# Performance work log

Measured on AMD Instinct MI355X. Metric: run time of the kernel, lower is better.

Reference implementation:

```python
import jax, jax.numpy as jnp
import numpy as np
from jax.experimental.ode import odeint

DIM = 768
BATCH = 2048
T = 32
W_SCALE = 0.02  # small init so dynamics are smooth for the adaptive solver


def setup_inputs() -> dict:
    key = jax.random.key(0)
    k = jax.random.split(key, 8)
    f32 = jnp.float32
    return {
        "x": jax.random.normal(k[0], (BATCH, DIM), f32),
        "t_span": (jnp.arange(T, dtype=f32) * 0.1),  # monotone increasing time grid
        # dynamics_net: Linear(dim, 2*dim) -> tanh -> Linear(2*dim, dim)
        "W1": jax.random.normal(k[1], (DIM, 2 * DIM), f32) * W_SCALE,
        "b1": jnp.zeros((2 * DIM,), f32),
        "W2": jax.random.normal(k[2], (2 * DIM, DIM), f32) * W_SCALE,
        "b2": jnp.zeros((DIM,), f32),
        # memory_net: Linear(dim, dim) -> tanh
        "Wm": jax.random.normal(k[3], (DIM, DIM), f32) * W_SCALE,
        "bm": jnp.zeros((DIM,), f32),
    }


def reference(x, t_span, W1, b1, W2, b2, Wm, bm):
    """Adaptive dopri5 integration of dE/dt = dynamics_net(E) + memory_net(E).

    Returns the emotional trajectory with shape [time, batch, dim], matching
    torchdiffeq.odeint(..., method='dopri5').
    """

    def f(y, t, W1, b1, W2, b2, Wm, bm):
        # dynamics_net(y): tanh MLP 768 -> 1536 -> 768
        dyn = jnp.tanh(y @ W1 + b1) @ W2 + b2
        # memory_net(y): tanh(Linear(768 -> 768))
        mem = jnp.tanh(y @ Wm + bm)
        return dyn + mem

    # jax's odeint is an adaptive dopri5 solver (same scheme as torchdiffeq dopri5).
    traj = odeint(f, x, t_span, W1, b1, W2, b2, Wm, bm, rtol=1e-5, atol=1e-6)
    return traj  # [T, BATCH, DIM]
```

## Files before the change

### kernel.cpp

```cpp
#include <hip/hip_runtime.h>
#include <math.h>

#define DIM   768
#define HID   1536
#define NCAT  2304
#define BATCH 2048
#define NELEM (BATCH * DIM)

typedef _Float16 f16x8 __attribute__((ext_vector_type(8)));
typedef _Float16 f16x4 __attribute__((ext_vector_type(4)));
typedef float f32x4 __attribute__((ext_vector_type(4)));

__device__ __forceinline__ float fast_tanh(float x) {
  float e = __expf(2.0f * x);
  return 1.0f - 2.0f / (e + 1.0f);
}

#define AS1 __attribute__((address_space(1)))
#define AS3 __attribute__((address_space(3)))
__device__ __forceinline__ void gload_lds16(const void* g, void* l) {
  __builtin_amdgcn_global_load_lds((const AS1 unsigned int*)g,
                                   (AS3 unsigned int*)l, 16, 0, 0);
}

template <int ROWS>
__device__ __forceinline__ void stage_tile(const _Float16* __restrict__ g,
                                           int K, char* lds, int w, int l) {
  constexpr int NCH = ROWS / 8;
  const int sub  = l >> 3;
  const int slot = (l & 7) ^ sub;
#pragma unroll
  for (int i = 0; i < NCH / 4; ++i) {
    const int j = w + i * 4;
    const int row = j * 8 + sub;
    gload_lds16(g + (size_t)row * K + slot * 8, lds + j * 1024);
  }
}

__device__ __forceinline__ f16x8 ldfrag(const char* base, int row, int kk,
                                        int lq) {
  const int slot = (kk * 4 + lq) ^ (row & 7);
  return *reinterpret_cast<const f16x8*>(base + row * 128 + slot * 16);
}

template <int MODE, int BM, int BN, int KITERS>
__global__ __launch_bounds__(256, (MODE == 0) ? 3 : 2) void gemm_k(
    const _Float16* __restrict__ A, const _Float16* __restrict__ Bt,
    const float* __restrict__ bias, _Float16* __restrict__ Hout,
    float* __restrict__ kmem, const float* __restrict__ b2,
    float* __restrict__ y, float* __restrict__ accb,
    _Float16* __restrict__ ts, float* __restrict__ out_row,
    const float* __restrict__ tg, int step, float hmul, int initf) {
  constexpr int K = KITERS * 64;
  constexpr int WM = BM / 32;
  constexpr int WN = BN / 32;
  constexpr int BUF = (BM + BN) * 128;
  constexpr int NBUF = (MODE == 0) ? 2 : 3;
  constexpr int SISS = BM / 32 + BN / 32;
  __shared__ __align__(16) char smem[NBUF * BUF];

  const int tid = threadIdx.x;
  const int w = tid >> 6, l = tid & 63;
  const int lr = l & 15, lq = l >> 4;
  const int m0 = blockIdx.y * BM;
  const int n0 = blockIdx.x * BN;
  const int wr = (w >> 1) * (WM * 16);
  const int wc = (w & 1) * (WN * 16);

  const _Float16* Ag = A + (size_t)m0 * K;
  const _Float16* Bg = Bt + (size_t)n0 * K;

  f32x4 acc[WM][WN];
#pragma unroll
  for (int m = 0; m < WM; ++m)
#pragma unroll
    for (int n = 0; n < WN; ++n) acc[m][n] = f32x4{0.f, 0.f, 0.f, 0.f};

  auto STAGE = [&](int t) {
    char* base = smem + (t % NBUF) * BUF;
    stage_tile<BM>(Ag + t * 64, K, base, w, l);
    stage_tile<BN>(Bg + t * 64, K, base + BM * 128, w, l);
  };

  STAGE(0);
  if (NBUF == 3 && KITERS > 1) STAGE(1);

  for (int kt = 0; kt < KITERS; ++kt) {
    if (NBUF == 2 && kt + 1 < KITERS) STAGE(kt + 1);
    if (kt + 1 < KITERS)
      asm volatile("s_waitcnt vmcnt(%0)" ::"n"(SISS) : "memory");
    else
      asm volatile("s_waitcnt vmcnt(0)" ::: "memory");
    __builtin_amdgcn_s_barrier();
    __builtin_amdgcn_sched_barrier(0);
    if (NBUF == 3 && kt + 2 < KITERS) STAGE(kt + 2);

    const char* As = smem + (kt % NBUF) * BUF;
    const char* Bs = As + BM * 128;
#pragma unroll
    for (int kk = 0; kk < 2; ++kk) {
      f16x8 afr[WM], bfr[WN];
#pragma unroll
      for (int n = 0; n < WN; ++n) bfr[n] = ldfrag(Bs, wc + n * 16 + lr, kk, lq);
#pragma unroll
      for (int m = 0; m < WM; ++m) afr[m] = ldfrag(As, wr + m * 16 + lr, kk, lq);
      __builtin_amdgcn_s_setprio(1);
#pragma unroll
      for (int m = 0; m < WM; ++m)
#pragma unroll
        for (int n = 0; n < WN; ++n)
          acc[m][n] = __builtin_amdgcn_mfma_f32_16x16x32_f16(afr[m], bfr[n],
                                                             acc[m][n], 0, 0, 0);
      __builtin_amdgcn_s_setprio(0);
    }
    if (NBUF == 2) __builtin_amdgcn_s_barrier();
  }

  if (MODE == 0) {
#pragma unroll
    for (int m = 0; m < WM; ++m)
#pragma unroll
      for (int n = 0; n < WN; ++n) {
        const int gcol = n0 + wc + n * 16 + lr;
        const float bv = bias[gcol];
#pragma unroll
        for (int j = 0; j < 4; ++j) {
          const int grow = m0 + wr + m * 16 + lq * 4 + j;
          const float t = fast_tanh(acc[m][n][j] + bv);
          if (gcol < HID)
            Hout[(size_t)grow * HID + gcol] = (_Float16)t;
          else
            kmem[(size_t)grow * DIM + (gcol - HID)] = t;
        }
      }
  } else {
    const float h = tg[step + 1] - tg[step];
#pragma unroll
    for (int m = 0; m < WM; ++m)
#pragma unroll
      for (int n = 0; n < WN; ++n) {
        const int gcol = n0 + wc + n * 16 + lr;
        const float bv = b2[gcol];
#pragma unroll
        for (int j = 0; j < 4; ++j) {
          const int grow = m0 + wr + m * 16 + lq * 4 + j;
          const size_t idx = (size_t)grow * DIM + gcol;
          const float kv = acc[m][n][j] + kmem[idx] + bv;
          if (MODE == 1) {
            const float av = initf ? kv : (accb[idx] + 2.0f * kv);
            accb[idx] = av;
            const float tv = y[idx] + (hmul * h) * kv;
            ts[idx] = (_Float16)tv;
          } else {
            const float v = y[idx] + (h * (1.0f / 6.0f)) * (accb[idx] + kv);
            y[idx] = v;
            out_row[idx] = v;
            ts[idx] = (_Float16)v;
          }
        }
      }
  }
}

__global__ __launch_bounds__(256) void init_k(
    const float* __restrict__ x, float* __restrict__ y,
    float* __restrict__ out0, _Float16* __restrict__ ys) {
  const int i4 = blockIdx.x * 256 + threadIdx.x;
  const int base = i4 * 4;
  f32x4 v = *(const f32x4*)(x + base);
  *(f32x4*)(y + base) = v;
  *(f32x4*)(out0 + base) = v;
  f16x4 hv;
#pragma unroll
  for (int j = 0; j < 4; ++j) hv[j] = (_Float16)v[j];
  *(f16x4*)(ys + base) = hv;
}

__global__ __launch_bounds__(256) void prep_wcat_k(
    const float* __restrict__ W1, const float* __restrict__ Wm,
    _Float16* __restrict__ out) {
  const int idx = blockIdx.x * 256 + threadIdx.x;
  const int nrow = idx / DIM, k = idx % DIM;
  const float v = (nrow < HID) ? W1[(size_t)k * HID + nrow]
                               : Wm[(size_t)k * DIM + (nrow - HID)];
  out[idx] = (_Float16)v;
}
__global__ __launch_bounds__(256) void prep_w2t_k(
    const float* __restrict__ W2, _Float16* __restrict__ out) {
  const int idx = blockIdx.x * 256 + threadIdx.x;
  const int nrow = idx / HID, k = idx % HID;
  out[idx] = (_Float16)W2[(size_t)k * DIM + nrow];
}
__global__ __launch_bounds__(256) void prep_bias_k(
    const float* __restrict__ b1, const float* __restrict__ bmv,
    float* __restrict__ out) {
  const int i = blockIdx.x * 256 + threadIdx.x;
  if (i < NCAT) out[i] = (i < HID) ? b1[i] : bmv[i - HID];
}

extern "C" void kernel_launch(void* const* d_in, const int* in_sizes, int n_in,
                              void* d_out, int out_size, void* d_ws,
                              size_t ws_size, hipStream_t stream) {
  const float* x  = (const float*)d_in[0];
  const float* tg = (const float*)d_in[1];
  const float* W1 = (const float*)d_in[2];
  const float* b1 = (const float*)d_in[3];
  const float* W2 = (const float*)d_in[4];
  const float* b2 = (const float*)d_in[5];
  const float* Wm = (const float*)d_in[6];
  const float* bm = (const float*)d_in[7];
  float* out = (float*)d_out;
  const int T = in_sizes[1];

  float* y        = (float*)d_ws;
  float* accb     = y + NELEM;
  float* kmem     = accb + NELEM;
  float* bias_cat = kmem + NELEM;
  _Float16* ys    = (_Float16*)(bias_cat + NCAT);
  _Float16* ts    = ys + NELEM;
  _Float16* Hh    = ts + NELEM;
  _Float16* WcatT = Hh + (size_t)BATCH * HID;
  _Float16* W2T   = WcatT + (size_t)NCAT * DIM;

  prep_wcat_k<<<(NCAT * DIM) / 256, 256, 0, stream>>>(W1, Wm, WcatT);
  prep_w2t_k<<<(DIM * HID) / 256, 256, 0, stream>>>(W2, W2T);
  prep_bias_k<<<(NCAT + 255) / 256, 256, 0, stream>>>(b1, bm, bias_cat);
  init_k<<<NELEM / 1024, 256, 0, stream>>>(x, y, out, ys);

  const dim3 g0(NCAT / 96, BATCH / 64);
  const dim3 g1(DIM / 96, BATCH / 32);

  auto gemm0 = [&](const _Float16* a) {
    gemm_k<0, 64, 96, 12><<<g0, 256, 0, stream>>>(
        a, WcatT, bias_cat, Hh, kmem, nullptr, nullptr, nullptr, nullptr,
        nullptr, nullptr, 0, 0.f, 0);
  };
  auto gemm1_stage = [&](int step, float hmul, int initf) {
    gemm_k<1, 32, 96, 24><<<g1, 256, 0, stream>>>(
        Hh, W2T, nullptr, nullptr, kmem, b2, y, accb, ts, nullptr, tg, step,
        hmul, initf);
  };
  auto gemm1_final = [&](int step, float* orow) {
    gemm_k<2, 32, 96, 24><<<g1, 256, 0, stream>>>(
        Hh, W2T, nullptr, nullptr, kmem, b2, y, accb, ys, orow, tg, step, 0.f,
        0);
  };

  for (int i = 0; i < T - 1; ++i) {
    gemm0(ys);  gemm1_stage(i, 0.5f, 1);
    gemm0(ts);  gemm1_stage(i, 0.5f, 0);
    gemm0(ts);  gemm1_stage(i, 1.0f, 0);
    gemm0(ts);  gemm1_final(i, out + (size_t)(i + 1) * NELEM);
  }
}
```

Before: 4.178 ms.

## Store kmem/accb in fp16, remap blocks per XCD, enlarge second GEMM tile

```diff
diff --git a/kernel.cpp b/kernel.cpp
--- a/kernel.cpp
+++ b/kernel.cpp
@@ -44,11 +44,11 @@
 }
 
 template <int MODE, int BM, int BN, int KITERS>
-__global__ __launch_bounds__(256, (MODE == 0) ? 3 : 2) void gemm_k(
+__global__ __launch_bounds__(256, (MODE == 0) ? 3 : 1) void gemm_k(
     const _Float16* __restrict__ A, const _Float16* __restrict__ Bt,
     const float* __restrict__ bias, _Float16* __restrict__ Hout,
-    float* __restrict__ kmem, const float* __restrict__ b2,
-    float* __restrict__ y, float* __restrict__ accb,
+    _Float16* __restrict__ kmem, const float* __restrict__ b2,
+    float* __restrict__ y, _Float16* __restrict__ accb,
     _Float16* __restrict__ ts, float* __restrict__ out_row,
     const float* __restrict__ tg, int step, float hmul, int initf) {
   constexpr int K = KITERS * 64;
@@ -62,8 +62,19 @@
   const int tid = threadIdx.x;
   const int w = tid >> 6, l = tid & 63;
   const int lr = l & 15, lq = l >> 4;
-  const int m0 = blockIdx.y * BM;
-  const int n0 = blockIdx.x * BN;
+
+  const int flat = blockIdx.x;
+  const int xcd = flat & 7, slot = flat >> 3;
+  int mt, nt;
+  if (MODE == 0) {
+    mt = (xcd & 1) * 16 + (slot & 15);
+    nt = (xcd >> 1) * 6 + (slot >> 4);
+  } else {
+    mt = (xcd & 3) * 8 + (slot & 7);
+    nt = (xcd >> 2) * 4 + (slot >> 3);
+  }
+  const int m0 = mt * BM;
+  const int n0 = nt * BN;
   const int wr = (w >> 1) * (WM * 16);
   const int wc = (w & 1) * (WN * 16);
 
@@ -130,7 +141,7 @@
           if (gcol < HID)
             Hout[(size_t)grow * HID + gcol] = (_Float16)t;
           else
-            kmem[(size_t)grow * DIM + (gcol - HID)] = t;
+            kmem[(size_t)grow * DIM + (gcol - HID)] = (_Float16)t;
         }
       }
   } else {
@@ -145,14 +156,15 @@
         for (int j = 0; j < 4; ++j) {
           const int grow = m0 + wr + m * 16 + lq * 4 + j;
           const size_t idx = (size_t)grow * DIM + gcol;
-          const float kv = acc[m][n][j] + kmem[idx] + bv;
+          const float kv = acc[m][n][j] + (float)kmem[idx] + bv;
           if (MODE == 1) {
-            const float av = initf ? kv : (accb[idx] + 2.0f * kv);
-            accb[idx] = av;
+            const float av = initf ? kv : ((float)accb[idx] + 2.0f * kv);
+            accb[idx] = (_Float16)av;
             const float tv = y[idx] + (hmul * h) * kv;
             ts[idx] = (_Float16)tv;
           } else {
-            const float v = y[idx] + (h * (1.0f / 6.0f)) * (accb[idx] + kv);
+            const float v =
+                y[idx] + (h * (1.0f / 6.0f)) * ((float)accb[idx] + kv);
             y[idx] = v;
             out_row[idx] = v;
             ts[idx] = (_Float16)v;
@@ -213,10 +225,10 @@
   const int T = in_sizes[1];
 
   float* y        = (float*)d_ws;
-  float* accb     = y + NELEM;
-  float* kmem     = accb + NELEM;
-  float* bias_cat = kmem + NELEM;
-  _Float16* ys    = (_Float16*)(bias_cat + NCAT);
+  float* bias_cat = y + NELEM;
+  _Float16* kmem  = (_Float16*)(bias_cat + NCAT);
+  _Float16* accb  = kmem + NELEM;
+  _Float16* ys    = accb + NELEM;
   _Float16* ts    = ys + NELEM;
   _Float16* Hh    = ts + NELEM;
   _Float16* WcatT = Hh + (size_t)BATCH * HID;
@@ -227,21 +239,18 @@
   prep_bias_k<<<(NCAT + 255) / 256, 256, 0, stream>>>(b1, bm, bias_cat);
   init_k<<<NELEM / 1024, 256, 0, stream>>>(x, y, out, ys);
 
-  const dim3 g0(NCAT / 96, BATCH / 64);
-  const dim3 g1(DIM / 96, BATCH / 32);
-
   auto gemm0 = [&](const _Float16* a) {
-    gemm_k<0, 64, 96, 12><<<g0, 256, 0, stream>>>(
+    gemm_k<0, 64, 96, 12><<<768, 256, 0, stream>>>(
         a, WcatT, bias_cat, Hh, kmem, nullptr, nullptr, nullptr, nullptr,
         nullptr, nullptr, 0, 0.f, 0);
   };
   auto gemm1_stage = [&](int step, float hmul, int initf) {
-    gemm_k<1, 32, 96, 24><<<g1, 256, 0, stream>>>(
+    gemm_k<1, 64, 96, 24><<<256, 256, 0, stream>>>(
         Hh, W2T, nullptr, nullptr, kmem, b2, y, accb, ts, nullptr, tg, step,
         hmul, initf);
   };
   auto gemm1_final = [&](int step, float* orow) {
-    gemm_k<2, 32, 96, 24><<<g1, 256, 0, stream>>>(
+    gemm_k<2, 64, 96, 24><<<256, 256, 0, stream>>>(
         Hh, W2T, nullptr, nullptr, kmem, b2, y, accb, ys, orow, tg, step, 0.f,
         0);
   };
```

Measured after the change: 4.380 ms. 1.05x slower.
